# Optimization experiments

Measured on AMD Instinct MI355X. Metric: run time of the kernel, lower is better.

Reference implementation:

```python
import jax, jax.numpy as jnp
import numpy as np

EMBED_DIM = 1280
NUM_HEADS = 20
HEAD_DIM = EMBED_DIM // NUM_HEADS  # 64
TGT_LEN = 2048
BSZ = 2
SCALING = HEAD_DIM ** -0.5


def setup_inputs() -> dict:
    key = jax.random.key(0)
    ks = jax.random.split(key, 6)
    s = EMBED_DIM ** -0.5
    query = jax.random.normal(ks[0], (TGT_LEN, BSZ, EMBED_DIM), dtype=jnp.float32)
    Wq = jax.random.normal(ks[1], (EMBED_DIM, EMBED_DIM), dtype=jnp.float32) * s
    Wk = jax.random.normal(ks[2], (EMBED_DIM, EMBED_DIM), dtype=jnp.float32) * s
    Wv = jax.random.normal(ks[3], (EMBED_DIM, EMBED_DIM), dtype=jnp.float32) * s
    Wo = jax.random.normal(ks[4], (EMBED_DIM, EMBED_DIM), dtype=jnp.float32) * s
    bq = jnp.zeros((EMBED_DIM,), jnp.float32)
    bk = jnp.zeros((EMBED_DIM,), jnp.float32)
    bv = jnp.zeros((EMBED_DIM,), jnp.float32)
    bo = jnp.zeros((EMBED_DIM,), jnp.float32)
    # key_padding_mask: (bsz, src_len), True = padded; pad last 256 keys of batch 1
    kpm = np.zeros((BSZ, TGT_LEN), dtype=bool)
    kpm[1, -256:] = True
    key_padding_mask = jnp.asarray(kpm)
    return {"query": query, "key_padding_mask": key_padding_mask,
            "Wq": Wq, "bq": bq, "Wk": Wk, "bk": bk,
            "Wv": Wv, "bv": bv, "Wo": Wo, "bo": bo}


def _mha(query, key_padding_mask, Wq, bq, Wk, bk, Wv, bv, Wo, bo):
    T, B, E = query.shape
    H, D = NUM_HEADS, HEAD_DIM
    q = (query @ Wq + bq) * SCALING            # [T, B, E]
    k = query @ Wk + bk
    v = query @ Wv + bv
    # reshape to [B*H, T, D] as in the TF code
    q = q.reshape(T, B * H, D).transpose(1, 0, 2)
    k = k.reshape(T, B * H, D).transpose(1, 0, 2)
    v = v.reshape(T, B * H, D).transpose(1, 0, 2)
    attn_weights = jnp.einsum('bqd,bkd->bqk', q, k)   # [B*H, T, T]
    # key padding mask: (B, src_len), 1s excluded -> -inf
    aw = attn_weights.reshape(B, H, T, T)
    aw = jnp.where(key_padding_mask[:, None, None, :], -jnp.inf, aw)
    attn_weights_float = jax.nn.softmax(aw.astype(jnp.float32).reshape(B * H, T, T), axis=-1)
    attn_probs = attn_weights_float.astype(v.dtype)  # dropout rate 0.0 -> identity
    attn = jnp.einsum('bqk,bkd->bqd', attn_probs, v)  # [B*H, T, D]
    attn = attn.transpose(1, 0, 2).reshape(T, B, E)
    attn = attn @ Wo + bo
    # need_weights=True (default), need_head_weights=False -> mean over heads
    avg_weights = attn_weights_float.reshape(B, H, T, T).transpose(1, 0, 2, 3).mean(axis=0)
    return attn, avg_weights


def reference(query, key_padding_mask, Wq, bq, Wk, bk, Wv, bv, Wo, bo):
    return _mha(query, key_padding_mask, Wq, bq, Wk, bk, Wv, bv, Wo, bo)
```

## Files before the change

### kernel.cpp

```cpp
#include <hip/hip_runtime.h>

#define T_LEN 2048
#define BSZ   2
#define EMB   1280
#define NH    20
#define HD    64
#define NBH   (BSZ*NH)
#define NR    (T_LEN*BSZ)
#define QSCALE (0.125f * 1.4426950408889634f)

typedef short bf16x8 __attribute__((ext_vector_type(8)));
typedef short bf16x4 __attribute__((ext_vector_type(4)));
typedef float f32x4  __attribute__((ext_vector_type(4)));

__device__ inline short f2bf(float f) {
    union { float f; unsigned u; } v; v.f = f;
    unsigned u = v.u + 0x7FFF + ((v.u >> 16) & 1);
    return (short)(u >> 16);
}

__device__ inline unsigned cvt_pk_bf16(float lo, float hi) {
    unsigned r;
    asm("v_cvt_pk_bf16_f32 %0, %1, %2" : "=v"(r) : "v"(lo), "v"(hi));
    return r;
}

__global__ __launch_bounds__(256) void k_cvt_x(
    const float* __restrict__ X, short* __restrict__ Xb)
{
    size_t i0 = ((size_t)blockIdx.x*256 + threadIdx.x) * 8;
    float4 a = *(const float4*)(X + i0);
    float4 b = *(const float4*)(X + i0 + 4);
    bf16x8 r = { f2bf(a.x), f2bf(a.y), f2bf(a.z), f2bf(a.w),
                 f2bf(b.x), f2bf(b.y), f2bf(b.z), f2bf(b.w) };
    *(bf16x8*)(Xb + i0) = r;
}

__global__ __launch_bounds__(256) void k_cvt_wt(
    const float* __restrict__ Wq, const float* __restrict__ Wk,
    const float* __restrict__ Wv, const float* __restrict__ Wo,
    short* __restrict__ Wqt, short* __restrict__ Wkt,
    short* __restrict__ Wvt, short* __restrict__ Wot)
{
    const int z = blockIdx.z;
    const float* __restrict__ W = (z==0)?Wq:(z==1)?Wk:(z==2)?Wv:Wo;
    short* __restrict__ Wt      = (z==0)?Wqt:(z==1)?Wkt:(z==2)?Wvt:Wot;

    const int k0 = blockIdx.y * 32;
    const int n0 = blockIdx.x * 32;
    const int t  = threadIdx.x;

    __shared__ float Ls[32][33];
    {
        int row = t >> 3, col = (t & 7) * 4;
        *(float4*)&Ls[row][col] = *(const float4*)(W + (size_t)(k0+row)*EMB + n0 + col);
    }
    __syncthreads();
    {
        int n = t >> 3, k4 = (t & 7) * 4;
        bf16x4 r = { f2bf(Ls[k4+0][n]), f2bf(Ls[k4+1][n]),
                     f2bf(Ls[k4+2][n]), f2bf(Ls[k4+3][n]) };
        *(bf16x4*)(Wt + (size_t)(n0+n)*EMB + k0 + k4) = r;
    }
}

__global__ __launch_bounds__(256) void k_gemm_qkv(
    const short* __restrict__ Xb,
    const short* __restrict__ Wqt, const short* __restrict__ Wkt, const short* __restrict__ Wvt,
    const float* __restrict__ bq, const float* __restrict__ bk, const float* __restrict__ bv,
    short* __restrict__ Qb, short* __restrict__ Kb, short* __restrict__ Vt)
{
    const int which = blockIdx.z;
    const short* __restrict__ Wt   = (which==0) ? Wqt : (which==1) ? Wkt : Wvt;
    const float* __restrict__ bias = (which==0) ? bq  : (which==1) ? bk  : bv;
    const float scale = (which==0) ? QSCALE : 1.0f;

    const int bm = blockIdx.y * 128;
    const int bn = blockIdx.x * 128;
    const int t    = threadIdx.x;
    const int wave = t >> 6, lane = t & 63;
    const int l16  = lane & 15, quad = lane >> 4;
    const int wm   = (wave >> 1) * 64, wn = (wave & 1) * 64;

    __shared__ short As[128][72];
    __shared__ short Bs[128][72];

    f32x4 acc[4][4] = {};

    for (int kt = 0; kt < EMB; kt += 64) {
        __syncthreads();
        const short* Ag = Xb + (size_t)bm*EMB + kt;
        const short* Bg = Wt + (size_t)bn*EMB + kt;
        #pragma unroll
        for (int c = 0; c < 4; ++c) {
            int idx = c*256 + t;
            int row = idx >> 3, col8 = (idx & 7) * 8;
            *(bf16x8*)&As[row][col8] = *(const bf16x8*)(Ag + (size_t)row*EMB + col8);
            *(bf16x8*)&Bs[row][col8] = *(const bf16x8*)(Bg + (size_t)row*EMB + col8);
        }
        __syncthreads();
        #pragma unroll
        for (int ks = 0; ks < 64; ks += 32) {
            bf16x8 af[4], bfr[4];
            #pragma unroll
            for (int mi=0;mi<4;++mi) af[mi]  = *(const bf16x8*)&As[wm + mi*16 + l16][ks + quad*8];
            #pragma unroll
            for (int ni=0;ni<4;++ni) bfr[ni] = *(const bf16x8*)&Bs[wn + ni*16 + l16][ks + quad*8];
            #pragma unroll
            for (int mi=0;mi<4;++mi)
                #pragma unroll
                for (int ni=0;ni<4;++ni)
                    acc[mi][ni] = __builtin_amdgcn_mfma_f32_16x16x32_bf16(af[mi], bfr[ni], acc[mi][ni], 0,0,0);
        }
    }

    #pragma unroll
    for (int ni=0;ni<4;++ni) {
        int c = bn + wn + ni*16 + l16;
        float bval = bias[c];
        int h = c >> 6, d = c & 63;
        #pragma unroll
        for (int mi=0;mi<4;++mi) {
            #pragma unroll
            for (int j=0;j<4;++j) {
                int r = bm + wm + mi*16 + quad*4 + j;
                int tt = r >> 1, bb = r & 1;
                float val = (acc[mi][ni][j] + bval) * scale;
                if (which == 2)
                    Vt[((size_t)(bb*NH+h)*HD + d)*T_LEN + tt] = f2bf(val);
                else {
                    short* dst = (which==0) ? Qb : Kb;
                    dst[((size_t)(bb*NH+h)*T_LEN + tt)*HD + d] = f2bf(val);
                }
            }
        }
    }
}

__global__ __launch_bounds__(256) void k_pv(
    const short* __restrict__ Qb, const short* __restrict__ Kb, const short* __restrict__ Vt,
    const int* __restrict__ kpm,
    float* __restrict__ Linv,
    short* __restrict__ AttnMidb)
{
    const int qt = blockIdx.x;
    const int bh = blockIdx.y;
    const int b  = bh / NH, h = bh % NH;
    const int t    = threadIdx.x;
    const int w    = t >> 6;
    const int lane = t & 63;
    const int l16  = lane & 15;
    const int quad = lane >> 4;
    const int q0   = qt*128 + w*32;

    __shared__ short Ks[2][64][72];
    __shared__ short Vts[2][64][72];
    __shared__ float MfL[2][64];
    __shared__ float Lsh[128];

    bf16x8 qf[2][2];
    #pragma unroll
    for (int mi=0;mi<2;++mi)
        #pragma unroll
        for (int ch=0;ch<2;++ch)
            qf[mi][ch] = *(const bf16x8*)(Qb + ((size_t)bh*T_LEN + q0 + mi*16 + l16)*HD + ch*32 + quad*8);

    const int row0 = t >> 3, col8 = (t & 7) * 8;
    const short* Kgb = Kb + (size_t)bh*T_LEN*HD;
    const short* Vgb = Vt + (size_t)bh*HD*T_LEN;

    *(bf16x8*)&Ks[0][row0][col8]      = *(const bf16x8*)(Kgb + (size_t)row0*HD + col8);
    *(bf16x8*)&Ks[0][row0+32][col8]   = *(const bf16x8*)(Kgb + (size_t)(row0+32)*HD + col8);
    *(bf16x8*)&Vts[0][row0][col8]     = *(const bf16x8*)(Vgb + (size_t)row0*T_LEN + col8);
    *(bf16x8*)&Vts[0][row0+32][col8]  = *(const bf16x8*)(Vgb + (size_t)(row0+32)*T_LEN + col8);
    if (t < 64) MfL[0][t] = kpm[b*T_LEN + t] ? 0.f : 1.f;
    __syncthreads();

    f32x4 o[2][4] = {};
    float l[2] = {0.f, 0.f};
    int cur = 0;

    for (int kt = 0; kt < T_LEN; kt += 64) {
        const int ktn = kt + 64;
        const bool has_next = ktn < T_LEN;
        const int nxt = cur ^ 1;

        bf16x8 kr0, kr1, vr0, vr1;
        float mfn = 0.f;
        if (has_next) {
            kr0 = *(const bf16x8*)(Kgb + (size_t)(ktn + row0)*HD + col8);
            kr1 = *(const bf16x8*)(Kgb + (size_t)(ktn + row0 + 32)*HD + col8);
            vr0 = *(const bf16x8*)(Vgb + (size_t)row0*T_LEN + ktn + col8);
            vr1 = *(const bf16x8*)(Vgb + (size_t)(row0+32)*T_LEN + ktn + col8);
            if (t < 64) mfn = kpm[b*T_LEN + ktn + t] ? 0.f : 1.f;
        }

        f32x4 s[4][2] = {};
        #pragma unroll
        for (int ch = 0; ch < 2; ++ch) {
            bf16x8 ka[4];
            #pragma unroll
            for (int mb=0;mb<4;++mb) ka[mb] = *(const bf16x8*)&Ks[cur][mb*16 + l16][ch*32 + quad*8];
            #pragma unroll
            for (int mb=0;mb<4;++mb)
                #pragma unroll
                for (int mi=0;mi<2;++mi)
                    s[mb][mi] = __builtin_amdgcn_mfma_f32_16x16x32_bf16(ka[mb], qf[mi][ch], s[mb][mi], 0,0,0);
        }

        unsigned pu[2][2][4];
        #pragma unroll
        for (int c = 0; c < 2; ++c) {
            #pragma unroll
            for (int mb2 = 0; mb2 < 2; ++mb2) {
                const int mb = c*2 + mb2;
                float4 mf = *(const float4*)&MfL[cur][mb*16 + quad*4];
                #pragma unroll
                for (int mi = 0; mi < 2; ++mi) {
                    float p0 = __builtin_amdgcn_exp2f(s[mb][mi][0]) * mf.x;
                    float p1 = __builtin_amdgcn_exp2f(s[mb][mi][1]) * mf.y;
                    float p2 = __builtin_amdgcn_exp2f(s[mb][mi][2]) * mf.z;
                    float p3 = __builtin_amdgcn_exp2f(s[mb][mi][3]) * mf.w;
                    l[mi] += (p0 + p1) + (p2 + p3);
                    pu[c][mi][mb2*2+0] = cvt_pk_bf16(p0, p1);
                    pu[c][mi][mb2*2+1] = cvt_pk_bf16(p2, p3);
                }
            }
        }

        if (has_next) {
            *(bf16x8*)&Ks[nxt][row0][col8]      = kr0;
            *(bf16x8*)&Ks[nxt][row0+32][col8]   = kr1;
            *(bf16x8*)&Vts[nxt][row0][col8]     = vr0;
            *(bf16x8*)&Vts[nxt][row0+32][col8]  = vr1;
            if (t < 64) MfL[nxt][t] = mfn;
        }

        #pragma unroll
        for (int c = 0; c < 2; ++c) {
            bf16x8 vv[4];
            #pragma unroll
            for (int nb=0;nb<4;++nb) {
                bf16x4 va = *(const bf16x4*)&Vts[cur][nb*16 + l16][c*32 + quad*4];
                bf16x4 vb = *(const bf16x4*)&Vts[cur][nb*16 + l16][c*32 + 16 + quad*4];
                vv[nb] = (bf16x8){va[0],va[1],va[2],va[3], vb[0],vb[1],vb[2],vb[3]};
            }
            #pragma unroll
            for (int mi=0;mi<2;++mi) {
                union { unsigned u[4]; bf16x8 v; } pa;
                pa.u[0]=pu[c][mi][0]; pa.u[1]=pu[c][mi][1];
                pa.u[2]=pu[c][mi][2]; pa.u[3]=pu[c][mi][3];
                #pragma unroll
                for (int nb=0;nb<4;++nb)
                    o[mi][nb] = __builtin_amdgcn_mfma_f32_16x16x32_bf16(pa.v, vv[nb], o[mi][nb], 0,0,0);
            }
        }

        __syncthreads();
        cur = nxt;
    }

    #pragma unroll
    for (int mi=0;mi<2;++mi) {
        l[mi] += __shfl_xor(l[mi], 16);
        l[mi] += __shfl_xor(l[mi], 32);
        float linv = 1.0f / l[mi];
        if (quad == 0) {
            Linv[(size_t)bh*T_LEN + q0 + mi*16 + l16] = linv;
            Lsh[w*32 + mi*16 + l16] = linv;
        }
    }
    #pragma unroll
    for (int mi=0;mi<2;++mi) {
        float4 li = *(const float4*)&Lsh[w*32 + mi*16 + quad*4];
        float lr[4] = {li.x, li.y, li.z, li.w};
        #pragma unroll
        for (int r=0;r<4;++r) {
            int q = q0 + mi*16 + quad*4 + r;
            size_t base = ((size_t)q*BSZ + b)*EMB + h*HD;
            #pragma unroll
            for (int nb=0;nb<4;++nb)
                AttnMidb[base + nb*16 + l16] = f2bf(o[mi][nb][r] * lr[r]);
        }
    }
}

__global__ __launch_bounds__(256) void k_meanw(
    const short* __restrict__ Qb, const short* __restrict__ Kb,
    const int* __restrict__ kpm,
    const float* __restrict__ Linv,
    float* __restrict__ avg)
{
    const int kt = blockIdx.x;
    const int qt = blockIdx.y;
    const int b  = blockIdx.z;
    const int t    = threadIdx.x;
    const int wave = t >> 6, lane = t & 63;
    const int l16  = lane & 15, quad = lane >> 4;

    __shared__ short Qs[64][72];
    __shared__ short Ks[64][72];
    __shared__ float Lish[64];
    __shared__ int   msk[64];

    if (t < 64) msk[t] = kpm[b*T_LEN + kt*64 + t];

    f32x4 acc[4] = {};
    const int qrow_in = wave*16 + quad*4;

    for (int h = 0; h < NH; ++h) {
        const int bh = b*NH + h;
        __syncthreads();
        {
            const short* Qg = Qb + ((size_t)bh*T_LEN + qt*64)*HD;
            const short* Kg = Kb + ((size_t)bh*T_LEN + kt*64)*HD;
            #pragma unroll
            for (int c = 0; c < 2; ++c) {
                int idx = c*256 + t;
                int row = idx >> 3, col8 = (idx & 7) * 8;
                *(bf16x8*)&Qs[row][col8] = *(const bf16x8*)(Qg + (size_t)row*HD + col8);
                *(bf16x8*)&Ks[row][col8] = *(const bf16x8*)(Kg + (size_t)row*HD + col8);
            }
        }
        if (t < 64) Lish[t] = Linv[(size_t)bh*T_LEN + qt*64 + t];
        __syncthreads();

        bf16x8 aq0 = *(const bf16x8*)&Qs[wave*16 + l16][quad*8];
        bf16x8 aq1 = *(const bf16x8*)&Qs[wave*16 + l16][32 + quad*8];

        float lv[4];
        #pragma unroll
        for (int r = 0; r < 4; ++r)
            lv[r] = Lish[qrow_in + r] * (1.0f/NH);

        #pragma unroll
        for (int nb = 0; nb < 4; ++nb) {
            bf16x8 bk0 = *(const bf16x8*)&Ks[nb*16 + l16][quad*8];
            bf16x8 bk1 = *(const bf16x8*)&Ks[nb*16 + l16][32 + quad*8];
            f32x4 s = {};
            s = __builtin_amdgcn_mfma_f32_16x16x32_bf16(aq0, bk0, s, 0,0,0);
            s = __builtin_amdgcn_mfma_f32_16x16x32_bf16(aq1, bk1, s, 0,0,0);
            const bool mk = msk[nb*16 + l16] != 0;
            #pragma unroll
            for (int r = 0; r < 4; ++r)
                acc[nb][r] += mk ? 0.f : __builtin_amdgcn_exp2f(s[r]) * lv[r];
        }
    }

    #pragma unroll
    for (int r = 0; r < 4; ++r) {
        int q = qt*64 + qrow_in + r;
        size_t base = ((size_t)b*T_LEN + q) * T_LEN + (size_t)kt*64;
        #pragma unroll
        for (int nb = 0; nb < 4; ++nb)
            avg[base + nb*16 + l16] = acc[nb][r];
    }
}

__global__ __launch_bounds__(256) void k_gemm_out(
    const short* __restrict__ Ab, const short* __restrict__ Wot,
    const float* __restrict__ bo, float* __restrict__ out)
{
    const int bm = blockIdx.y * 128;
    const int bn = blockIdx.x * 128;
    const int t    = threadIdx.x;
    const int wave = t >> 6, lane = t & 63;
    const int l16  = lane & 15, quad = lane >> 4;
    const int wm   = (wave >> 1) * 64, wn = (wave & 1) * 64;

    __shared__ short As[128][72];
    __shared__ short Bs[128][72];

    f32x4 acc[4][4] = {};

    for (int kt = 0; kt < EMB; kt += 64) {
        __syncthreads();
        const short* Ag = Ab  + (size_t)bm*EMB + kt;
        const short* Bg = Wot + (size_t)bn*EMB + kt;
        #pragma unroll
        for (int c = 0; c < 4; ++c) {
            int idx = c*256 + t;
            int row = idx >> 3, col8 = (idx & 7) * 8;
            *(bf16x8*)&As[row][col8] = *(const bf16x8*)(Ag + (size_t)row*EMB + col8);
            *(bf16x8*)&Bs[row][col8] = *(const bf16x8*)(Bg + (size_t)row*EMB + col8);
        }
        __syncthreads();
        #pragma unroll
        for (int ks = 0; ks < 64; ks += 32) {
            bf16x8 af[4], bfr[4];
            #pragma unroll
            for (int mi=0;mi<4;++mi) af[mi]  = *(const bf16x8*)&As[wm + mi*16 + l16][ks + quad*8];
            #pragma unroll
            for (int ni=0;ni<4;++ni) bfr[ni] = *(const bf16x8*)&Bs[wn + ni*16 + l16][ks + quad*8];
            #pragma unroll
            for (int mi=0;mi<4;++mi)
                #pragma unroll
                for (int ni=0;ni<4;++ni)
                    acc[mi][ni] = __builtin_amdgcn_mfma_f32_16x16x32_bf16(af[mi], bfr[ni], acc[mi][ni], 0,0,0);
        }
    }

    #pragma unroll
    for (int ni=0;ni<4;++ni) {
        int c = bn + wn + ni*16 + l16;
        float bval = bo[c];
        #pragma unroll
        for (int mi=0;mi<4;++mi) {
            #pragma unroll
            for (int j=0;j<4;++j) {
                int r = bm + wm + mi*16 + quad*4 + j;
                out[(size_t)r*EMB + c] = acc[mi][ni][j] + bval;
            }
        }
    }
}

extern "C" void kernel_launch(void* const* d_in, const int* in_sizes, int n_in,
                              void* d_out, int out_size, void* d_ws, size_t ws_size,
                              hipStream_t stream) {
    const float* X   = (const float*)d_in[0];
    const int*   kpm = (const int*)  d_in[1];
    const float* Wq  = (const float*)d_in[2];
    const float* bq  = (const float*)d_in[3];
    const float* Wk  = (const float*)d_in[4];
    const float* bk  = (const float*)d_in[5];
    const float* Wv  = (const float*)d_in[6];
    const float* bv  = (const float*)d_in[7];
    const float* Wo  = (const float*)d_in[8];
    const float* bo  = (const float*)d_in[9];

    float* out = (float*)d_out;
    float* ws  = (float*)d_ws;

    const size_t QKV = (size_t)NBH * T_LEN * HD;
    float* Linv = ws;
    short* Xb   = (short*)(Linv + (size_t)NBH * T_LEN);
    short* Wqt  = Xb  + (size_t)NR * EMB;
    short* Wkt  = Wqt + (size_t)EMB * EMB;
    short* Wvt  = Wkt + (size_t)EMB * EMB;
    short* Wot  = Wvt + (size_t)EMB * EMB;
    short* Qb   = Wot + (size_t)EMB * EMB;
    short* Kb   = Qb  + QKV;
    short* Vt   = Kb  + QKV;
    short* Amid = Vt  + QKV;

    float* attn_out = out;
    float* avg      = out + (size_t)T_LEN * BSZ * EMB;

    k_cvt_x   <<<dim3((NR*EMB)/(256*8)), 256, 0, stream>>>(X, Xb);
    k_cvt_wt  <<<dim3(EMB/32, EMB/32, 4), 256, 0, stream>>>(Wq, Wk, Wv, Wo, Wqt, Wkt, Wvt, Wot);
    k_gemm_qkv<<<dim3(EMB/128, NR/128, 3), 256, 0, stream>>>(Xb, Wqt, Wkt, Wvt, bq, bk, bv, Qb, Kb, Vt);
    k_pv      <<<dim3(T_LEN/128, NBH),   256, 0, stream>>>(Qb, Kb, Vt, kpm, Linv, Amid);
    k_meanw   <<<dim3(T_LEN/64, T_LEN/64, BSZ), 256, 0, stream>>>(Qb, Kb, kpm, Linv, avg);
    k_gemm_out<<<dim3(EMB/128, NR/128),  256, 0, stream>>>(Amid, Wot, bo, attn_out);
}
```

Before: 357.0 us.

## Use direct global-to-LDS loads in GEMMs and split k_pv across 8 waves

```diff
diff --git a/kernel.cpp b/kernel.cpp
--- a/kernel.cpp
+++ b/kernel.cpp
@@ -25,6 +25,13 @@
     return r;
 }
 
+__device__ inline void glds16(const short* g, short* l) {
+    __builtin_amdgcn_global_load_lds(
+        (const __attribute__((address_space(1))) void*)g,
+        (__attribute__((address_space(3))) void*)l,
+        16, 0, 0);
+}
+
 __global__ __launch_bounds__(256) void k_cvt_x(
     const float* __restrict__ X, short* __restrict__ Xb)
 {
@@ -82,8 +89,11 @@
     const int l16  = lane & 15, quad = lane >> 4;
     const int wm   = (wave >> 1) * 64, wn = (wave & 1) * 64;
 
-    __shared__ short As[128][72];
-    __shared__ short Bs[128][72];
+    __shared__ short As[128][64];
+    __shared__ short Bs[128][64];
+
+    const int srow = lane >> 3;
+    const int scol = (lane & 7) * 8;
 
     f32x4 acc[4][4] = {};
 
@@ -93,10 +103,10 @@
         const short* Bg = Wt + (size_t)bn*EMB + kt;
         #pragma unroll
         for (int c = 0; c < 4; ++c) {
-            int idx = c*256 + t;
-            int row = idx >> 3, col8 = (idx & 7) * 8;
-            *(bf16x8*)&As[row][col8] = *(const bf16x8*)(Ag + (size_t)row*EMB + col8);
-            *(bf16x8*)&Bs[row][col8] = *(const bf16x8*)(Bg + (size_t)row*EMB + col8);
+            int seg = wave*4 + c;
+            int grow = seg*8 + srow;
+            glds16(Ag + (size_t)grow*EMB + scol, &As[seg*8][0]);
+            glds16(Bg + (size_t)grow*EMB + scol, &Bs[seg*8][0]);
         }
         __syncthreads();
         #pragma unroll
@@ -137,7 +147,7 @@
     }
 }
 
-__global__ __launch_bounds__(256) void k_pv(
+__global__ __launch_bounds__(512) void k_pv(
     const short* __restrict__ Qb, const short* __restrict__ Kb, const short* __restrict__ Vt,
     const int* __restrict__ kpm,
     float* __restrict__ Linv,
@@ -151,33 +161,29 @@
     const int lane = t & 63;
     const int l16  = lane & 15;
     const int quad = lane >> 4;
-    const int q0   = qt*128 + w*32;
+    const int q0   = qt*128 + w*16;
 
     __shared__ short Ks[2][64][72];
     __shared__ short Vts[2][64][72];
     __shared__ float MfL[2][64];
     __shared__ float Lsh[128];
 
-    bf16x8 qf[2][2];
+    bf16x8 qf[2];
     #pragma unroll
-    for (int mi=0;mi<2;++mi)
-        #pragma unroll
-        for (int ch=0;ch<2;++ch)
-            qf[mi][ch] = *(const bf16x8*)(Qb + ((size_t)bh*T_LEN + q0 + mi*16 + l16)*HD + ch*32 + quad*8);
+    for (int ch=0;ch<2;++ch)
+        qf[ch] = *(const bf16x8*)(Qb + ((size_t)bh*T_LEN + q0 + l16)*HD + ch*32 + quad*8);
 
     const int row0 = t >> 3, col8 = (t & 7) * 8;
     const short* Kgb = Kb + (size_t)bh*T_LEN*HD;
     const short* Vgb = Vt + (size_t)bh*HD*T_LEN;
 
-    *(bf16x8*)&Ks[0][row0][col8]      = *(const bf16x8*)(Kgb + (size_t)row0*HD + col8);
-    *(bf16x8*)&Ks[0][row0+32][col8]   = *(const bf16x8*)(Kgb + (size_t)(row0+32)*HD + col8);
-    *(bf16x8*)&Vts[0][row0][col8]     = *(const bf16x8*)(Vgb + (size_t)row0*T_LEN + col8);
-    *(bf16x8*)&Vts[0][row0+32][col8]  = *(const bf16x8*)(Vgb + (size_t)(row0+32)*T_LEN + col8);
+    *(bf16x8*)&Ks[0][row0][col8]  = *(const bf16x8*)(Kgb + (size_t)row0*HD + col8);
+    *(bf16x8*)&Vts[0][row0][col8] = *(const bf16x8*)(Vgb + (size_t)row0*T_LEN + col8);
     if (t < 64) MfL[0][t] = kpm[b*T_LEN + t] ? 0.f : 1.f;
     __syncthreads();
 
-    f32x4 o[2][4] = {};
-    float l[2] = {0.f, 0.f};
+    f32x4 o[4] = {};
+    float l = 0.f;
     int cur = 0;
 
     for (int kt = 0; kt < T_LEN; kt += 64) {
@@ -185,17 +191,15 @@
         const bool has_next = ktn < T_LEN;
         const int nxt = cur ^ 1;
 
-        bf16x8 kr0, kr1, vr0, vr1;
+        bf16x8 kr0, vr0;
         float mfn = 0.f;
         if (has_next) {
             kr0 = *(const bf16x8*)(Kgb + (size_t)(ktn + row0)*HD + col8);
-            kr1 = *(const bf16x8*)(Kgb + (size_t)(ktn + row0 + 32)*HD + col8);
             vr0 = *(const bf16x8*)(Vgb + (size_t)row0*T_LEN + ktn + col8);
-            vr1 = *(const bf16x8*)(Vgb + (size_t)(row0+32)*T_LEN + ktn + col8);
             if (t < 64) mfn = kpm[b*T_LEN + ktn + t] ? 0.f : 1.f;
         }
 
-        f32x4 s[4][2] = {};
+        f32x4 s[4] = {};
         #pragma unroll
         for (int ch = 0; ch < 2; ++ch) {
             bf16x8 ka[4];
@@ -203,36 +207,29 @@
             for (int mb=0;mb<4;++mb) ka[mb] = *(const bf16x8*)&Ks[cur][mb*16 + l16][ch*32 + quad*8];
             #pragma unroll
             for (int mb=0;mb<4;++mb)
-                #pragma unroll
-                for (int mi=0;mi<2;++mi)
-                    s[mb][mi] = __builtin_amdgcn_mfma_f32_16x16x32_bf16(ka[mb], qf[mi][ch], s[mb][mi], 0,0,0);
-        }
-
-        unsigned pu[2][2][4];
+                s[mb] = __builtin_amdgcn_mfma_f32_16x16x32_bf16(ka[mb], qf[ch], s[mb], 0,0,0);
+        }
+
+        unsigned pu[2][4];
         #pragma unroll
         for (int c = 0; c < 2; ++c) {
             #pragma unroll
             for (int mb2 = 0; mb2 < 2; ++mb2) {
                 const int mb = c*2 + mb2;
                 float4 mf = *(const float4*)&MfL[cur][mb*16 + quad*4];
-                #pragma unroll
-                for (int mi = 0; mi < 2; ++mi) {
-                    float p0 = __builtin_amdgcn_exp2f(s[mb][mi][0]) * mf.x;
-                    float p1 = __builtin_amdgcn_exp2f(s[mb][mi][1]) * mf.y;
-                    float p2 = __builtin_amdgcn_exp2f(s[mb][mi][2]) * mf.z;
-                    float p3 = __builtin_amdgcn_exp2f(s[mb][mi][3]) * mf.w;
-                    l[mi] += (p0 + p1) + (p2 + p3);
-                    pu[c][mi][mb2*2+0] = cvt_pk_bf16(p0, p1);
-                    pu[c][mi][mb2*2+1] = cvt_pk_bf16(p2, p3);
-                }
+                float p0 = __builtin_amdgcn_exp2f(s[mb][0]) * mf.x;
+                float p1 = __builtin_amdgcn_exp2f(s[mb][1]) * mf.y;
+                float p2 = __builtin_amdgcn_exp2f(s[mb][2]) * mf.z;
+                float p3 = __builtin_amdgcn_exp2f(s[mb][3]) * mf.w;
+                l += (p0 + p1) + (p2 + p3);
+                pu[c][mb2*2+0] = cvt_pk_bf16(p0, p1);
+                pu[c][mb2*2+1] = cvt_pk_bf16(p2, p3);
             }
         }
 
         if (has_next) {
-            *(bf16x8*)&Ks[nxt][row0][col8]      = kr0;
-            *(bf16x8*)&Ks[nxt][row0+32][col8]   = kr1;
-            *(bf16x8*)&Vts[nxt][row0][col8]     = vr0;
-            *(bf16x8*)&Vts[nxt][row0+32][col8]  = vr1;
+            *(bf16x8*)&Ks[nxt][row0][col8]  = kr0;
+            *(bf16x8*)&Vts[nxt][row0][col8] = vr0;
             if (t < 64) MfL[nxt][t] = mfn;
         }
 
@@ -245,42 +242,35 @@
                 bf16x4 vb = *(const bf16x4*)&Vts[cur][nb*16 + l16][c*32 + 16 + quad*4];
                 vv[nb] = (bf16x8){va[0],va[1],va[2],va[3], vb[0],vb[1],vb[2],vb[3]};
             }
-            #pragma unroll
-            for (int mi=0;mi<2;++mi) {
-                union { unsigned u[4]; bf16x8 v; } pa;
-                pa.u[0]=pu[c][mi][0]; pa.u[1]=pu[c][mi][1];
-                pa.u[2]=pu[c][mi][2]; pa.u[3]=pu[c][mi][3];
-                #pragma unroll
-                for (int nb=0;nb<4;++nb)
-                    o[mi][nb] = __builtin_amdgcn_mfma_f32_16x16x32_bf16(pa.v, vv[nb], o[mi][nb], 0,0,0);
-            }
+            union { unsigned u[4]; bf16x8 v; } pa;
+            pa.u[0]=pu[c][0]; pa.u[1]=pu[c][1];
+            pa.u[2]=pu[c][2]; pa.u[3]=pu[c][3];
+            #pragma unroll
+            for (int nb=0;nb<4;++nb)
+                o[nb] = __builtin_amdgcn_mfma_f32_16x16x32_bf16(pa.v, vv[nb], o[nb], 0,0,0);
         }
 
         __syncthreads();
         cur = nxt;
     }
 
-    #pragma unroll
-    for (int mi=0;mi<2;++mi) {
-        l[mi] += __shfl_xor(l[mi], 16);
-        l[mi] += __shfl_xor(l[mi], 32);
-        float linv = 1.0f / l[mi];
-        if (quad == 0) {
-            Linv[(size_t)bh*T_LEN + q0 + mi*16 + l16] = linv;
-            Lsh[w*32 + mi*16 + l16] = linv;
-        }
-    }
-    #pragma unroll
-    for (int mi=0;mi<2;++mi) {
-        float4 li = *(const float4*)&Lsh[w*32 + mi*16 + quad*4];
+    l += __shfl_xor(l, 16);
+    l += __shfl_xor(l, 32);
+    float linv = 1.0f / l;
+    if (quad == 0) {
+        Linv[(size_t)bh*T_LEN + q0 + l16] = linv;
+        Lsh[w*16 + l16] = linv;
+    }
+    {
+        float4 li = *(const float4*)&Lsh[w*16 + quad*4];
         float lr[4] = {li.x, li.y, li.z, li.w};
         #pragma unroll
         for (int r=0;r<4;++r) {
-            int q = q0 + mi*16 + quad*4 + r;
+            int q = q0 + quad*4 + r;
             size_t base = ((size_t)q*BSZ + b)*EMB + h*HD;
             #pragma unroll
             for (int nb=0;nb<4;++nb)
-                AttnMidb[base + nb*16 + l16] = f2bf(o[mi][nb][r] * lr[r]);
+                AttnMidb[base + nb*16 + l16] = f2bf(o[nb][r] * lr[r]);
         }
     }
 }
@@ -368,8 +358,11 @@
     const int l16  = lane & 15, quad = lane >> 4;
     const int wm   = (wave >> 1) * 64, wn = (wave & 1) * 64;
 
-    __shared__ short As[128][72];
-    __shared__ short Bs[128][72];
+    __shared__ short As[128][64];
+    __shared__ short Bs[128][64];
+
+    const int srow = lane >> 3;
+    const int scol = (lane & 7) * 8;
 
     f32x4 acc[4][4] = {};
 
@@ -379,10 +372,10 @@
         const short* Bg = Wot + (size_t)bn*EMB + kt;
         #pragma unroll
         for (int c = 0; c < 4; ++c) {
-            int idx = c*256 + t;
-            int row = idx >> 3, col8 = (idx & 7) * 8;
-            *(bf16x8*)&As[row][col8] = *(const bf16x8*)(Ag + (size_t)row*EMB + col8);
-            *(bf16x8*)&Bs[row][col8] = *(const bf16x8*)(Bg + (size_t)row*EMB + col8);
+            int seg = wave*4 + c;
+            int grow = seg*8 + srow;
+            glds16(Ag + (size_t)grow*EMB + scol, &As[seg*8][0]);
+            glds16(Bg + (size_t)grow*EMB + scol, &Bs[seg*8][0]);
         }
         __syncthreads();
         #pragma unroll
@@ -450,7 +443,7 @@
     k_cvt_x   <<<dim3((NR*EMB)/(256*8)), 256, 0, stream>>>(X, Xb);
     k_cvt_wt  <<<dim3(EMB/32, EMB/32, 4), 256, 0, stream>>>(Wq, Wk, Wv, Wo, Wqt, Wkt, Wvt, Wot);
     k_gemm_qkv<<<dim3(EMB/128, NR/128, 3), 256, 0, stream>>>(Xb, Wqt, Wkt, Wvt, bq, bk, bv, Qb, Kb, Vt);
-    k_pv      <<<dim3(T_LEN/128, NBH),   256, 0, stream>>>(Qb, Kb, Vt, kpm, Linv, Amid);
+    k_pv      <<<dim3(T_LEN/128, NBH),   512, 0, stream>>>(Qb, Kb, Vt, kpm, Linv, Amid);
     k_meanw   <<<dim3(T_LEN/64, T_LEN/64, BSZ), 256, 0, stream>>>(Qb, Kb, kpm, Linv, avg);
     k_gemm_out<<<dim3(EMB/128, NR/128),  256, 0, stream>>>(Amid, Wot, bo, attn_out);
 }
```

Result: slower. 373.4 us (+4.6%).
